# Kernel tuning notes

Hardware: AMD Instinct MI355X
Metric: run time of the kernel (lower is better)

The kernel has to match this reference:

```python
import jax, jax.numpy as jnp
import numpy as np

LN_EPS = 1e-5
NORM_EPS = 1e-12


def entmax15_last(x):
    """Exact 1.5-entmax over the last axis (Peters & Martins sort algorithm)."""
    d = x.shape[-1]
    x = x / 2.0
    x = x - jnp.max(x, axis=-1, keepdims=True)
    xs = jnp.sort(x, axis=-1)[..., ::-1]  # descending
    k = jnp.arange(1, d + 1, dtype=x.dtype)
    mean = jnp.cumsum(xs, axis=-1) / k
    meansq = jnp.cumsum(xs * xs, axis=-1) / k
    ss = k * (meansq - jnp.square(mean))
    delta = (1.0 - ss) / k
    tau = mean - jnp.sqrt(jnp.clip(delta, 0.0))
    support = (tau <= xs).astype(jnp.int32)
    k_star = jnp.sum(support, axis=-1, keepdims=True) - 1  # last valid index
    tau_star = jnp.take_along_axis(tau, k_star, axis=-1)
    return jnp.square(jnp.maximum(x - tau_star, 0.0))


def layer_norm(x, gamma, beta):
    mu = jnp.mean(x, axis=-1, keepdims=True)
    var = jnp.mean(jnp.square(x - mu), axis=-1, keepdims=True)
    return (x - mu) / jnp.sqrt(var + LN_EPS) * gamma + beta


def setup_inputs() -> dict:
    key = jax.random.key(0)
    ks = jax.random.split(key, 4)
    B, M, N, D, T, L = 256, 64, 32, 128, 64, 128
    return {
        "x": jax.random.normal(ks[0], (B, M, D), dtype=jnp.float32),
        "route_weights": jax.random.normal(ks[1], (M, N, D, T), dtype=jnp.float32),
        "thread": jax.random.uniform(ks[2], (1, M, N), dtype=jnp.float32),
        "routing_leaves": jax.random.uniform(ks[3], (L, T), dtype=jnp.float32),
        "ln_gamma": jnp.ones((T,), dtype=jnp.float32),
        "ln_beta": jnp.zeros((T,), dtype=jnp.float32),
    }


def reference(x, route_weights, thread, routing_leaves, ln_gamma, ln_beta):
    # entmax15 over dim=-2 (the in_capsule_size axis D) of route_weights [M,N,D,T]
    w = jnp.swapaxes(route_weights, -1, -2)
    w = entmax15_last(w)
    weights = jnp.swapaxes(w, -1, -2)
    # priors: [B, M, N, T]
    priors = jnp.einsum('bmd,mndt->bmnt', x, weights)
    # routing
    leave_hash = routing_leaves / jnp.maximum(
        jnp.linalg.norm(routing_leaves, axis=-1, keepdims=True), NORM_EPS)
    votes = jax.nn.sigmoid(jnp.einsum('ld,bmnt->bmnl', leave_hash, priors)) if False else \
        jax.nn.sigmoid(jnp.einsum('ld,bmnd->bmnl', leave_hash, priors))  # [B,M,N,L]
    mean_cap = jnp.mean(votes, axis=1, keepdims=True)
    dis = jnp.mean(jnp.square(votes - mean_cap), axis=-1)  # [B,M,N]
    weight = jax.nn.relu(jnp.square(thread) - dis)
    prob = jax.nn.softmax(weight, axis=-2)  # over M (in capsules)
    next_caps = jnp.sum(prob[:, :, :, None] * priors, axis=1)  # [B,N,T]
    return layer_norm(next_caps, ln_gamma, ln_beta)
```

## Files before the change

kernel.cpp:

```cpp
#include <hip/hip_runtime.h>
#include <hip/hip_bf16.h>
#include <math.h>

#define B_ 256
#define M_ 64
#define N_ 32
#define D_ 128
#define T_ 64
#define L_ 128

typedef __attribute__((ext_vector_type(8))) short short8;
typedef __attribute__((ext_vector_type(4))) float floatx4;

__device__ __forceinline__ unsigned short f2bf(float f) {
  unsigned int u = __float_as_uint(f);
  unsigned int r = (u + 0x7fffu + ((u >> 16) & 1u)) >> 16;
  return (unsigned short)r;
}
__device__ __forceinline__ float bf2f(unsigned short s) {
  return __uint_as_float(((unsigned int)s) << 16);
}
__device__ __forceinline__ float frcp(float x) { return __builtin_amdgcn_rcpf(x); }

__global__ __launch_bounds__(256) void k_entmax(const float* __restrict__ rw,
                                                unsigned short* __restrict__ wq2,
                                                const float* __restrict__ x,
                                                const float* __restrict__ leaves,
                                                unsigned short* __restrict__ xb2,
                                                unsigned short* __restrict__ lhn,
                                                const float* __restrict__ thr,
                                                float* __restrict__ thrT) {
  const int tid = threadIdx.x;
  if (blockIdx.x >= 2048) {
    int bid = blockIdx.x - 2048;
    if (bid < 2048) {
      size_t e = ((size_t)bid * 256 + tid) * 4;
      int b = (int)(e >> 13);
      int rem = (int)(e & 8191);
      int mm = rem >> 7, dd = rem & 127;
      float4 v = *(const float4*)(x + e);
      ushort4 o;
      o.x = f2bf(v.x); o.y = f2bf(v.y); o.z = f2bf(v.z); o.w = f2bf(v.w);
      *(ushort4*)(xb2 + ((size_t)mm * B_ + b) * D_ + dd) = o;
    } else if (bid == 2048) {
      if (tid < L_) {
        const float* r = leaves + tid * T_;
        float ss = 0.f;
        for (int i = 0; i < T_; ++i) ss = fmaf(r[i], r[i], ss);
        float inv = frcp(fmaxf(sqrtf(ss), 1e-12f));
        unsigned short* o = lhn + tid * T_;
        for (int i = 0; i < T_; ++i) o[i] = f2bf(r[i] * inv);
      }
    } else {
#pragma unroll
      for (int k = 0; k < 8; ++k) {
        int idx = k * 256 + tid;
        int nn = idx >> 6, mm = idx & 63;
        thrT[idx] = thr[mm * N_ + nn];
      }
    }
    return;
  }

  const int gv = blockIdx.x * 64 + (tid >> 2);
  const int h = tid & 3;
  const int mn = gv >> 6;
  const int t = gv & 63;
  const float* base = rw + ((size_t)mn * D_ + h * 32) * T_ + t;
  float xv_[32];
#pragma unroll
  for (int i = 0; i < 32; ++i) xv_[i] = base[(size_t)i * T_];
  float mx = xv_[0];
#pragma unroll
  for (int i = 1; i < 32; ++i) mx = fmaxf(mx, xv_[i]);
  mx = fmaxf(mx, __shfl_xor(mx, 1));
  mx = fmaxf(mx, __shfl_xor(mx, 2));
#pragma unroll
  for (int i = 0; i < 32; ++i) xv_[i] = (xv_[i] - mx) * 0.5f;

  float lo = -1.0f, hi = 0.0f;
  for (int it = 0; it < 12; ++it) {
    float tau = 0.5f * (lo + hi);
    float f0 = 0.0f, f1 = 0.0f;
#pragma unroll
    for (int i = 0; i < 16; ++i) {
      float u0 = fmaxf(xv_[2 * i] - tau, 0.0f);
      float u1 = fmaxf(xv_[2 * i + 1] - tau, 0.0f);
      f0 = fmaf(u0, u0, f0);
      f1 = fmaf(u1, u1, f1);
    }
    float f = f0 + f1;
    f += __shfl_xor(f, 1);
    f += __shfl_xor(f, 2);
    if (f >= 1.0f) lo = tau; else hi = tau;
  }
  float tau0 = 0.5f * (lo + hi);
  float cnt = 0.f, s1 = 0.f, s2 = 0.f;
#pragma unroll
  for (int i = 0; i < 32; ++i) {
    bool in = xv_[i] > tau0;
    float q = in ? xv_[i] : 0.0f;
    cnt += in ? 1.0f : 0.0f;
    s1 += q;
    s2 = fmaf(q, q, s2);
  }
  cnt += __shfl_xor(cnt, 1); cnt += __shfl_xor(cnt, 2);
  s1 += __shfl_xor(s1, 1);   s1 += __shfl_xor(s1, 2);
  s2 += __shfl_xor(s2, 1);   s2 += __shfl_xor(s2, 2);
  float rc = frcp(cnt);
  float mean = s1 * rc;
  float ss = s2 - mean * s1;
  float delta = (1.0f - ss) * rc;
  float tau = mean - sqrtf(fmaxf(delta, 0.0f));

  unsigned short pv[32];
#pragma unroll
  for (int i = 0; i < 32; ++i) {
    float u = fmaxf(xv_[i] - tau, 0.0f);
    pv[i] = f2bf(u * u);
  }
  uint4* o = (uint4*)(wq2 + (size_t)gv * D_ + h * 32);
#pragma unroll
  for (int j = 0; j < 4; ++j) {
    uint4 w;
    w.x = (unsigned)pv[8 * j + 0] | ((unsigned)pv[8 * j + 1] << 16);
    w.y = (unsigned)pv[8 * j + 2] | ((unsigned)pv[8 * j + 3] << 16);
    w.z = (unsigned)pv[8 * j + 4] | ((unsigned)pv[8 * j + 5] << 16);
    w.w = (unsigned)pv[8 * j + 6] | ((unsigned)pv[8 * j + 7] << 16);
    o[j] = w;
  }
}

#define BS_STRIDE 136
__global__ __launch_bounds__(256, 4) void k_priors(const unsigned short* __restrict__ xb2,
                                                   const unsigned short* __restrict__ wq2,
                                                   unsigned short* __restrict__ priors) {
  const int m = blockIdx.x, n = blockIdx.y;
  const int tid = threadIdx.x;
  const int wid = tid >> 6, lane = tid & 63;
  const int row16 = lane & 15, quad = lane >> 4;
  __shared__ __align__(16) unsigned short Bs[64 * BS_STRIDE];
  __shared__ __align__(16) unsigned short Ct[128 * 72];

  const unsigned short* bsrc = wq2 + ((size_t)(m * N_ + n) * T_) * D_;
  {
    int tr = tid >> 4;
    int c = tid & 15;
#pragma unroll
    for (int p = 0; p < 4; ++p) {
      int row = p * 16 + tr;
      uint4 v = *(const uint4*)(bsrc + row * D_ + c * 8);
      *(uint4*)&Bs[row * BS_STRIDE + c * 8] = v;
    }
  }
  __syncthreads();

#pragma unroll
  for (int c = 0; c < 2; ++c) {
    short8 afr[2][4];
#pragma unroll
    for (int sc = 0; sc < 2; ++sc) {
      const int brow = c * 128 + wid * 32 + sc * 16 + row16;
      const unsigned short* aptr = xb2 + ((size_t)m * B_ + brow) * D_ + quad * 8;
#pragma unroll
      for (int ks = 0; ks < 4; ++ks) afr[sc][ks] = *(const short8*)(aptr + ks * 32);
    }

    floatx4 acc[2][4];
#pragma unroll
    for (int sc = 0; sc < 2; ++sc)
#pragma unroll
      for (int cf = 0; cf < 4; ++cf) acc[sc][cf] = (floatx4){0.f, 0.f, 0.f, 0.f};

#pragma unroll
    for (int cf = 0; cf < 4; ++cf) {
#pragma unroll
      for (int ks = 0; ks < 4; ++ks) {
        short8 bfr = *(const short8*)&Bs[(cf * 16 + row16) * BS_STRIDE + ks * 32 + quad * 8];
#pragma unroll
        for (int sc = 0; sc < 2; ++sc)
          acc[sc][cf] = __builtin_amdgcn_mfma_f32_16x16x32_bf16(afr[sc][ks], bfr, acc[sc][cf], 0, 0, 0);
      }
    }

    if (c) __syncthreads();
#pragma unroll
    for (int sc = 0; sc < 2; ++sc)
#pragma unroll
      for (int cf = 0; cf < 4; ++cf)
#pragma unroll
        for (int r = 0; r < 4; ++r)
          Ct[(wid * 32 + sc * 16 + quad * 4 + r) * 72 + cf * 16 + row16] = f2bf(acc[sc][cf][r]);
    __syncthreads();

    {
      int q = tid >> 4, s = tid & 15;
      int row = q * 8 + (s >> 1);
      int half = s & 1;
      const unsigned short* src = &Ct[row * 72 + half * 32];
      unsigned short* dst = priors +
          ((((size_t)n * 32 + c * 16 + q) * M_ + m) * 8 + (s >> 1)) * T_ + half * 32;
      uint4 a0 = *(const uint4*)(src);
      uint4 a1 = *(const uint4*)(src + 8);
      uint4 a2 = *(const uint4*)(src + 16);
      uint4 a3 = *(const uint4*)(src + 24);
      *(uint4*)(dst) = a0;
      *(uint4*)(dst + 8) = a1;
      *(uint4*)(dst + 16) = a2;
      *(uint4*)(dst + 24) = a3;
    }
  }
}

__global__ __launch_bounds__(256, 4) void k_route(const unsigned short* __restrict__ priors,
                                                  const unsigned short* __restrict__ lhn,
                                                  const float* __restrict__ thrT,
                                                  const float* __restrict__ gamma,
                                                  const float* __restrict__ beta,
                                                  float* __restrict__ out) {
  const int n = blockIdx.x, g4 = blockIdx.y;
  const int tid = threadIdx.x;
  const int wid = tid >> 6, lane = tid & 63;
  const int col = lane & 15, quad = lane >> 4;

  __shared__ float probL[4][64];

  const int g = g4 >> 1;
  const int bq = (g4 & 1) * 4 + wid;

  const unsigned short* base = priors + (((size_t)n * 32 + g) * M_) * 512 + bq * T_;
  short8 afr[4][2];
#pragma unroll
  for (int mt = 0; mt < 4; ++mt)
#pragma unroll
    for (int ks = 0; ks < 2; ++ks)
      afr[mt][ks] = *(const short8*)(base + (size_t)(mt * 16 + col) * 512 + ks * 32 + quad * 8);

  float thv = thrT[n * 64 + lane];

  float dis[4][4];
#pragma unroll
  for (int mt = 0; mt < 4; ++mt)
#pragma unroll
    for (int r = 0; r < 4; ++r) dis[mt][r] = 0.f;

#pragma unroll
  for (int s4 = 0; s4 < 4; ++s4) {
    floatx4 acc[4][2];
#pragma unroll
    for (int mt = 0; mt < 4; ++mt)
#pragma unroll
      for (int lt = 0; lt < 2; ++lt) acc[mt][lt] = (floatx4){0.f, 0.f, 0.f, 0.f};

#pragma unroll
    for (int lt = 0; lt < 2; ++lt) {
#pragma unroll
      for (int ks = 0; ks < 2; ++ks) {
        short8 bfr = *(const short8*)(lhn + (s4 * 32 + lt * 16 + col) * T_ + ks * 32 + quad * 8);
#pragma unroll
        for (int mt = 0; mt < 4; ++mt)
          acc[mt][lt] = __builtin_amdgcn_mfma_f32_16x16x32_bf16(afr[mt][ks], bfr, acc[mt][lt], 0, 0, 0);
      }
    }

#pragma unroll
    for (int mt = 0; mt < 4; ++mt)
#pragma unroll
      for (int lt = 0; lt < 2; ++lt)
#pragma unroll
        for (int r = 0; r < 4; ++r)
          acc[mt][lt][r] = frcp(1.0f + __expf(-acc[mt][lt][r]));

    float mc[2];
#pragma unroll
    for (int lt = 0; lt < 2; ++lt) {
      float s = 0.f;
#pragma unroll
      for (int mt = 0; mt < 4; ++mt)
#pragma unroll
        for (int r = 0; r < 4; ++r) s += acc[mt][lt][r];
      s += __shfl_xor(s, 16);
      s += __shfl_xor(s, 32);
      mc[lt] = s * (1.0f / 64.0f);
    }

#pragma unroll
    for (int mt = 0; mt < 4; ++mt)
#pragma unroll
      for (int r = 0; r < 4; ++r) {
        float s = 0.f;
#pragma unroll
        for (int lt = 0; lt < 2; ++lt) {
          float df = acc[mt][lt][r] - mc[lt];
          s = fmaf(df, df, s);
        }
        dis[mt][r] += s;
      }
  }

#pragma unroll
  for (int off = 1; off <= 8; off <<= 1)
#pragma unroll
    for (int mt = 0; mt < 4; ++mt)
#pragma unroll
      for (int r = 0; r < 4; ++r) dis[mt][r] += __shfl_xor(dis[mt][r], off);

  float e[4][4];
  float mxw = 0.f;
#pragma unroll
  for (int mt = 0; mt < 4; ++mt)
#pragma unroll
    for (int r = 0; r < 4; ++r) {
      float th = __shfl(thv, mt * 16 + quad * 4 + r);
      float w = fmaxf(th * th - dis[mt][r] * (1.0f / 128.0f), 0.0f);
      e[mt][r] = w;
      mxw = fmaxf(mxw, w);
    }
  mxw = fmaxf(mxw, __shfl_xor(mxw, 16));
  mxw = fmaxf(mxw, __shfl_xor(mxw, 32));
  float ssum = 0.f;
#pragma unroll
  for (int mt = 0; mt < 4; ++mt)
#pragma unroll
    for (int r = 0; r < 4; ++r) {
      e[mt][r] = __expf(e[mt][r] - mxw);
      ssum += e[mt][r];
    }
  ssum += __shfl_xor(ssum, 16);
  ssum += __shfl_xor(ssum, 32);
  float inv = frcp(ssum);
  if (col == 0) {
#pragma unroll
    for (int mt = 0; mt < 4; ++mt)
#pragma unroll
      for (int r = 0; r < 4; ++r)
        probL[wid][mt * 16 + quad * 4 + r] = e[mt][r] * inv;
  }

  float pr[4];
#pragma unroll
  for (int mt = 0; mt < 4; ++mt) pr[mt] = probL[wid][mt * 16 + col];

  float o[2][8];
#pragma unroll
  for (int ks = 0; ks < 2; ++ks)
#pragma unroll
    for (int j = 0; j < 8; ++j) o[ks][j] = 0.f;
#pragma unroll
  for (int mt = 0; mt < 4; ++mt)
#pragma unroll
    for (int ks = 0; ks < 2; ++ks)
#pragma unroll
      for (int j = 0; j < 8; ++j)
        o[ks][j] = fmaf(pr[mt], bf2f((unsigned short)afr[mt][ks][j]), o[ks][j]);
#pragma unroll
  for (int off = 1; off <= 8; off <<= 1)
#pragma unroll
    for (int ks = 0; ks < 2; ++ks)
#pragma unroll
      for (int j = 0; j < 8; ++j) o[ks][j] += __shfl_xor(o[ks][j], off);

  float mu = 0.f;
#pragma unroll
  for (int ks = 0; ks < 2; ++ks)
#pragma unroll
    for (int j = 0; j < 8; ++j) mu += o[ks][j];
  mu += __shfl_xor(mu, 16);
  mu += __shfl_xor(mu, 32);
  mu *= (1.0f / 64.0f);
  float var = 0.f;
#pragma unroll
  for (int ks = 0; ks < 2; ++ks)
#pragma unroll
    for (int j = 0; j < 8; ++j) {
      float d = o[ks][j] - mu;
      o[ks][j] = d;
      var = fmaf(d, d, var);
    }
  var += __shfl_xor(var, 16);
  var += __shfl_xor(var, 32);
  var *= (1.0f / 64.0f);
  float rstd = rsqrtf(var + 1e-5f);

  if (col == 0) {
    const int b = g4 * 4 + wid;
    float* obase = out + ((size_t)b * N_ + n) * T_;
#pragma unroll
    for (int ks = 0; ks < 2; ++ks) {
      int tb = ks * 32 + quad * 8;
      float4 g0 = *(const float4*)(gamma + tb);
      float4 g1 = *(const float4*)(gamma + tb + 4);
      float4 b0 = *(const float4*)(beta + tb);
      float4 b1 = *(const float4*)(beta + tb + 4);
      float4 r0, r1;
      r0.x = o[ks][0] * rstd * g0.x + b0.x;
      r0.y = o[ks][1] * rstd * g0.y + b0.y;
      r0.z = o[ks][2] * rstd * g0.z + b0.z;
      r0.w = o[ks][3] * rstd * g0.w + b0.w;
      r1.x = o[ks][4] * rstd * g1.x + b1.x;
      r1.y = o[ks][5] * rstd * g1.y + b1.y;
      r1.z = o[ks][6] * rstd * g1.z + b1.z;
      r1.w = o[ks][7] * rstd * g1.w + b1.w;
      *(float4*)(obase + tb) = r0;
      *(float4*)(obase + tb + 4) = r1;
    }
  }
}

extern "C" void kernel_launch(void* const* d_in, const int* in_sizes, int n_in,
                              void* d_out, int out_size, void* d_ws, size_t ws_size,
                              hipStream_t stream) {
  const float* x = (const float*)d_in[0];
  const float* rw = (const float*)d_in[1];
  const float* thr = (const float*)d_in[2];
  const float* leaves = (const float*)d_in[3];
  const float* gamma = (const float*)d_in[4];
  const float* beta = (const float*)d_in[5];
  float* out = (float*)d_out;

  char* ws = (char*)d_ws;
  unsigned short* wq2 = (unsigned short*)(ws);
  unsigned short* priors = (unsigned short*)(ws + 33554432);
  unsigned short* xb2 = (unsigned short*)(ws + 33554432 + 67108864);
  unsigned short* lhn = (unsigned short*)(ws + 100663296 + 4194304);
  float* thrT = (float*)(ws + 104857600 + 16384);

  hipLaunchKernelGGL(k_entmax, dim3(4098), dim3(256), 0, stream, rw, wq2, x, leaves, xb2, lhn, thr, thrT);
  hipLaunchKernelGGL(k_priors, dim3(64, 32), dim3(256), 0, stream, xb2, wq2, priors);
  hipLaunchKernelGGL(k_route, dim3(32, 64), dim3(256), 0, stream, priors, lhn, thrT, gamma, beta, out);
}
```

Measured before the change: 194.0 us.

## Compute transposed priors MFMA to write output directly, drop LDS staging

The priors GEMM swaps its operand roles: the weights tile held in LDS becomes the A operand and x becomes B. Each lane's accumulator then holds four contiguous T values, which are stored straight to global memory as ushort4, removing the Ct shared-memory transpose buffer and its barriers. Dropping Ct lowers LDS use, so the occupancy hint rises from 4 to 6 blocks. Separately, the entmax bisection is cut from 12 to 10 iterations, which saves compute but leaves a coarser starting threshold for the refinement step that follows. The direct stores are 8-byte and scattered rather than 16-byte coalesced, which may hurt write efficiency.

```diff
diff --git a/kernel.cpp b/kernel.cpp
--- a/kernel.cpp
+++ b/kernel.cpp
@@ -79,7 +79,7 @@
   for (int i = 0; i < 32; ++i) xv_[i] = (xv_[i] - mx) * 0.5f;
 
   float lo = -1.0f, hi = 0.0f;
-  for (int it = 0; it < 12; ++it) {
+  for (int it = 0; it < 10; ++it) {
     float tau = 0.5f * (lo + hi);
     float f0 = 0.0f, f1 = 0.0f;
 #pragma unroll
@@ -132,7 +132,7 @@
 }
 
 #define BS_STRIDE 136
-__global__ __launch_bounds__(256, 4) void k_priors(const unsigned short* __restrict__ xb2,
+__global__ __launch_bounds__(256, 6) void k_priors(const unsigned short* __restrict__ xb2,
                                                    const unsigned short* __restrict__ wq2,
                                                    unsigned short* __restrict__ priors) {
   const int m = blockIdx.x, n = blockIdx.y;
@@ -140,7 +140,6 @@
   const int wid = tid >> 6, lane = tid & 63;
   const int row16 = lane & 15, quad = lane >> 4;
   __shared__ __align__(16) unsigned short Bs[64 * BS_STRIDE];
-  __shared__ __align__(16) unsigned short Ct[128 * 72];
 
   const unsigned short* bsrc = wq2 + ((size_t)(m * N_ + n) * T_) * D_;
   {
@@ -155,59 +154,29 @@
   }
   __syncthreads();
 
-#pragma unroll
-  for (int c = 0; c < 2; ++c) {
-    short8 afr[2][4];
-#pragma unroll
-    for (int sc = 0; sc < 2; ++sc) {
-      const int brow = c * 128 + wid * 32 + sc * 16 + row16;
-      const unsigned short* aptr = xb2 + ((size_t)m * B_ + brow) * D_ + quad * 8;
-#pragma unroll
-      for (int ks = 0; ks < 4; ++ks) afr[sc][ks] = *(const short8*)(aptr + ks * 32);
-    }
-
-    floatx4 acc[2][4];
-#pragma unroll
-    for (int sc = 0; sc < 2; ++sc)
-#pragma unroll
-      for (int cf = 0; cf < 4; ++cf) acc[sc][cf] = (floatx4){0.f, 0.f, 0.f, 0.f};
-
+  const int b = wid * 64 + row16;
+#pragma unroll
+  for (int sub = 0; sub < 4; ++sub) {
+    const int bb = b + sub * 16;
+    const unsigned short* xptr = xb2 + ((size_t)m * B_ + bb) * D_ + quad * 8;
+    short8 bfr[4];
+#pragma unroll
+    for (int ks = 0; ks < 4; ++ks) bfr[ks] = *(const short8*)(xptr + ks * 32);
+
+    unsigned short* dstb = priors +
+        ((((size_t)n * 32 + (bb >> 3)) * M_ + m) * 8 + (bb & 7)) * T_ + quad * 4;
 #pragma unroll
     for (int cf = 0; cf < 4; ++cf) {
+      floatx4 acc = (floatx4){0.f, 0.f, 0.f, 0.f};
 #pragma unroll
       for (int ks = 0; ks < 4; ++ks) {
-        short8 bfr = *(const short8*)&Bs[(cf * 16 + row16) * BS_STRIDE + ks * 32 + quad * 8];
-#pragma unroll
-        for (int sc = 0; sc < 2; ++sc)
-          acc[sc][cf] = __builtin_amdgcn_mfma_f32_16x16x32_bf16(afr[sc][ks], bfr, acc[sc][cf], 0, 0, 0);
+        short8 afr = *(const short8*)&Bs[(cf * 16 + row16) * BS_STRIDE + ks * 32 + quad * 8];
+        acc = __builtin_amdgcn_mfma_f32_16x16x32_bf16(afr, bfr[ks], acc, 0, 0, 0);
       }
-    }
-
-    if (c) __syncthreads();
-#pragma unroll
-    for (int sc = 0; sc < 2; ++sc)
-#pragma unroll
-      for (int cf = 0; cf < 4; ++cf)
-#pragma unroll
-        for (int r = 0; r < 4; ++r)
-          Ct[(wid * 32 + sc * 16 + quad * 4 + r) * 72 + cf * 16 + row16] = f2bf(acc[sc][cf][r]);
-    __syncthreads();
-
-    {
-      int q = tid >> 4, s = tid & 15;
-      int row = q * 8 + (s >> 1);
-      int half = s & 1;
-      const unsigned short* src = &Ct[row * 72 + half * 32];
-      unsigned short* dst = priors +
-          ((((size_t)n * 32 + c * 16 + q) * M_ + m) * 8 + (s >> 1)) * T_ + half * 32;
-      uint4 a0 = *(const uint4*)(src);
-      uint4 a1 = *(const uint4*)(src + 8);
-      uint4 a2 = *(const uint4*)(src + 16);
-      uint4 a3 = *(const uint4*)(src + 24);
-      *(uint4*)(dst) = a0;
-      *(uint4*)(dst + 8) = a1;
-      *(uint4*)(dst + 16) = a2;
-      *(uint4*)(dst + 24) = a3;
+      ushort4 o4;
+      o4.x = f2bf(acc[0]); o4.y = f2bf(acc[1]);
+      o4.z = f2bf(acc[2]); o4.w = f2bf(acc[3]);
+      *(ushort4*)(dstb + cf * 16) = o4;
     }
   }
 }
```

Measured after the change: 211.9 us. 1.09x slower.

## Vectorize entmax loads over T, permute x/wq2 layouts, swap MFMA operands in priors

Applied to the files above, without the earlier changes.

The entmax kernel now has each thread load float4 vectors across four adjacent T columns and handle 16 D values, with an 8-lane shuffle reduction. The bisection is cut from 12 to 10 iterations, and stores are packed 16-element bf16 runs. The x conversion and the D-index layout of wq2 are permuted to match, and k_priors swaps its grid to n-major, preloads all x fragments, and swaps MFMA operands so the epilogue writes ushort4 to LDS. This aims at coalesced global reads of route_weights and fewer scalar LDS stores, at the cost of more registers and a reordered D axis that must stay consistent between the two kernels.

```diff
diff --git a/kernel.cpp b/kernel.cpp
--- a/kernel.cpp
+++ b/kernel.cpp
@@ -31,18 +31,25 @@
                                                 const float* __restrict__ thr,
                                                 float* __restrict__ thrT) {
   const int tid = threadIdx.x;
-  if (blockIdx.x >= 2048) {
-    int bid = blockIdx.x - 2048;
-    if (bid < 2048) {
-      size_t e = ((size_t)bid * 256 + tid) * 4;
-      int b = (int)(e >> 13);
-      int rem = (int)(e & 8191);
-      int mm = rem >> 7, dd = rem & 127;
-      float4 v = *(const float4*)(x + e);
-      ushort4 o;
-      o.x = f2bf(v.x); o.y = f2bf(v.y); o.z = f2bf(v.z); o.w = f2bf(v.w);
-      *(ushort4*)(xb2 + ((size_t)mm * B_ + b) * D_ + dd) = o;
-    } else if (bid == 2048) {
+  const int bx = blockIdx.x;
+  if (bx >= 1024) {
+    int bid = bx - 1024;
+    if (bid < 512) {
+      int idx = bid * 256 + tid;
+      int j = idx & 7, b = (idx >> 3) & 255, m = idx >> 11;
+      const float* xs = x + ((size_t)b * M_ + m) * D_ + j;
+      unsigned short pv[16];
+#pragma unroll
+      for (int i = 0; i < 16; ++i) pv[i] = f2bf(xs[i * 8]);
+      unsigned short* dst = xb2 + ((size_t)m * B_ + b) * D_ + j * 16;
+      uint4 w0, w1;
+      w0.x = pv[0] | ((unsigned)pv[1] << 16);  w0.y = pv[2] | ((unsigned)pv[3] << 16);
+      w0.z = pv[4] | ((unsigned)pv[5] << 16);  w0.w = pv[6] | ((unsigned)pv[7] << 16);
+      w1.x = pv[8] | ((unsigned)pv[9] << 16);  w1.y = pv[10] | ((unsigned)pv[11] << 16);
+      w1.z = pv[12] | ((unsigned)pv[13] << 16); w1.w = pv[14] | ((unsigned)pv[15] << 16);
+      *(uint4*)(dst) = w0;
+      *(uint4*)(dst + 8) = w1;
+    } else if (bid == 512) {
       if (tid < L_) {
         const float* r = leaves + tid * T_;
         float ss = 0.f;
@@ -62,72 +69,102 @@
     return;
   }
 
-  const int gv = blockIdx.x * 64 + (tid >> 2);
-  const int h = tid & 3;
-  const int mn = gv >> 6;
-  const int t = gv & 63;
-  const float* base = rw + ((size_t)mn * D_ + h * 32) * T_ + t;
-  float xv_[32];
-#pragma unroll
-  for (int i = 0; i < 32; ++i) xv_[i] = base[(size_t)i * T_];
-  float mx = xv_[0];
-#pragma unroll
-  for (int i = 1; i < 32; ++i) mx = fmaxf(mx, xv_[i]);
-  mx = fmaxf(mx, __shfl_xor(mx, 1));
-  mx = fmaxf(mx, __shfl_xor(mx, 2));
-#pragma unroll
-  for (int i = 0; i < 32; ++i) xv_[i] = (xv_[i] - mx) * 0.5f;
-
-  float lo = -1.0f, hi = 0.0f;
-  for (int it = 0; it < 12; ++it) {
-    float tau = 0.5f * (lo + hi);
-    float f0 = 0.0f, f1 = 0.0f;
+  const int mn = bx * 2 + (tid >> 7);
+  const int sub = tid & 127;
+  const int g = sub >> 3;
+  const int j = sub & 7;
+  const float* base = rw + (size_t)mn * D_ * T_ + g * 4;
+
+  floatx4 xv[16];
+#pragma unroll
+  for (int i = 0; i < 16; ++i)
+    xv[i] = *(const floatx4*)(base + (size_t)(i * 8 + j) * T_);
+
+  floatx4 mx = xv[0];
+#pragma unroll
+  for (int i = 1; i < 16; ++i)
+#pragma unroll
+    for (int c = 0; c < 4; ++c) mx[c] = fmaxf(mx[c], xv[i][c]);
+#pragma unroll
+  for (int off = 1; off <= 4; off <<= 1)
+#pragma unroll
+    for (int c = 0; c < 4; ++c) mx[c] = fmaxf(mx[c], __shfl_xor(mx[c], off));
+#pragma unroll
+  for (int i = 0; i < 16; ++i)
+#pragma unroll
+    for (int c = 0; c < 4; ++c) xv[i][c] = (xv[i][c] - mx[c]) * 0.5f;
+
+  floatx4 lo = (floatx4){-1.f, -1.f, -1.f, -1.f};
+  floatx4 hi = (floatx4){0.f, 0.f, 0.f, 0.f};
+  for (int it = 0; it < 10; ++it) {
+    floatx4 tau, f = (floatx4){0.f, 0.f, 0.f, 0.f};
+#pragma unroll
+    for (int c = 0; c < 4; ++c) tau[c] = 0.5f * (lo[c] + hi[c]);
+#pragma unroll
+    for (int i = 0; i < 16; ++i)
+#pragma unroll
+      for (int c = 0; c < 4; ++c) {
+        float u = fmaxf(xv[i][c] - tau[c], 0.0f);
+        f[c] = fmaf(u, u, f[c]);
+      }
+#pragma unroll
+    for (int off = 1; off <= 4; off <<= 1)
+#pragma unroll
+      for (int c = 0; c < 4; ++c) f[c] += __shfl_xor(f[c], off);
+#pragma unroll
+    for (int c = 0; c < 4; ++c) {
+      bool ge = f[c] >= 1.0f;
+      lo[c] = ge ? tau[c] : lo[c];
+      hi[c] = ge ? hi[c] : tau[c];
+    }
+  }
+  floatx4 tau0, cnt = (floatx4){0,0,0,0}, s1 = (floatx4){0,0,0,0}, s2 = (floatx4){0,0,0,0};
+#pragma unroll
+  for (int c = 0; c < 4; ++c) tau0[c] = 0.5f * (lo[c] + hi[c]);
+#pragma unroll
+  for (int i = 0; i < 16; ++i)
+#pragma unroll
+    for (int c = 0; c < 4; ++c) {
+      bool in = xv[i][c] > tau0[c];
+      float q = in ? xv[i][c] : 0.0f;
+      cnt[c] += in ? 1.0f : 0.0f;
+      s1[c] += q;
+      s2[c] = fmaf(q, q, s2[c]);
+    }
+#pragma unroll
+  for (int off = 1; off <= 4; off <<= 1)
+#pragma unroll
+    for (int c = 0; c < 4; ++c) {
+      cnt[c] += __shfl_xor(cnt[c], off);
+      s1[c] += __shfl_xor(s1[c], off);
+      s2[c] += __shfl_xor(s2[c], off);
+    }
+  floatx4 tau;
+#pragma unroll
+  for (int c = 0; c < 4; ++c) {
+    float rc = frcp(cnt[c]);
+    float mean = s1[c] * rc;
+    float ss = s2[c] - mean * s1[c];
+    float delta = (1.0f - ss) * rc;
+    tau[c] = mean - sqrtf(fmaxf(delta, 0.0f));
+  }
+
+#pragma unroll
+  for (int c = 0; c < 4; ++c) {
+    unsigned short pv[16];
 #pragma unroll
     for (int i = 0; i < 16; ++i) {
-      float u0 = fmaxf(xv_[2 * i] - tau, 0.0f);
-      float u1 = fmaxf(xv_[2 * i + 1] - tau, 0.0f);
-      f0 = fmaf(u0, u0, f0);
-      f1 = fmaf(u1, u1, f1);
-    }
-    float f = f0 + f1;
-    f += __shfl_xor(f, 1);
-    f += __shfl_xor(f, 2);
-    if (f >= 1.0f) lo = tau; else hi = tau;
-  }
-  float tau0 = 0.5f * (lo + hi);
-  float cnt = 0.f, s1 = 0.f, s2 = 0.f;
-#pragma unroll
-  for (int i = 0; i < 32; ++i) {
-    bool in = xv_[i] > tau0;
-    float q = in ? xv_[i] : 0.0f;
-    cnt += in ? 1.0f : 0.0f;
-    s1 += q;
-    s2 = fmaf(q, q, s2);
-  }
-  cnt += __shfl_xor(cnt, 1); cnt += __shfl_xor(cnt, 2);
-  s1 += __shfl_xor(s1, 1);   s1 += __shfl_xor(s1, 2);
-  s2 += __shfl_xor(s2, 1);   s2 += __shfl_xor(s2, 2);
-  float rc = frcp(cnt);
-  float mean = s1 * rc;
-  float ss = s2 - mean * s1;
-  float delta = (1.0f - ss) * rc;
-  float tau = mean - sqrtf(fmaxf(delta, 0.0f));
-
-  unsigned short pv[32];
-#pragma unroll
-  for (int i = 0; i < 32; ++i) {
-    float u = fmaxf(xv_[i] - tau, 0.0f);
-    pv[i] = f2bf(u * u);
-  }
-  uint4* o = (uint4*)(wq2 + (size_t)gv * D_ + h * 32);
-#pragma unroll
-  for (int j = 0; j < 4; ++j) {
-    uint4 w;
-    w.x = (unsigned)pv[8 * j + 0] | ((unsigned)pv[8 * j + 1] << 16);
-    w.y = (unsigned)pv[8 * j + 2] | ((unsigned)pv[8 * j + 3] << 16);
-    w.z = (unsigned)pv[8 * j + 4] | ((unsigned)pv[8 * j + 5] << 16);
-    w.w = (unsigned)pv[8 * j + 6] | ((unsigned)pv[8 * j + 7] << 16);
-    o[j] = w;
+      float u = fmaxf(xv[i][c] - tau[c], 0.0f);
+      pv[i] = f2bf(u * u);
+    }
+    unsigned short* dst = wq2 + ((size_t)mn * 64 + g * 4 + c) * D_ + j * 16;
+    uint4 w0, w1;
+    w0.x = pv[0] | ((unsigned)pv[1] << 16);  w0.y = pv[2] | ((unsigned)pv[3] << 16);
+    w0.z = pv[4] | ((unsigned)pv[5] << 16);  w0.w = pv[6] | ((unsigned)pv[7] << 16);
+    w1.x = pv[8] | ((unsigned)pv[9] << 16);  w1.y = pv[10] | ((unsigned)pv[11] << 16);
+    w1.z = pv[12] | ((unsigned)pv[13] << 16); w1.w = pv[14] | ((unsigned)pv[15] << 16);
+    *(uint4*)(dst) = w0;
+    *(uint4*)(dst + 8) = w1;
   }
 }
 
@@ -135,62 +172,67 @@
 __global__ __launch_bounds__(256, 4) void k_priors(const unsigned short* __restrict__ xb2,
                                                    const unsigned short* __restrict__ wq2,
                                                    unsigned short* __restrict__ priors) {
-  const int m = blockIdx.x, n = blockIdx.y;
+  const int n = blockIdx.x, m = blockIdx.y;
   const int tid = threadIdx.x;
   const int wid = tid >> 6, lane = tid & 63;
   const int row16 = lane & 15, quad = lane >> 4;
   __shared__ __align__(16) unsigned short Bs[64 * BS_STRIDE];
   __shared__ __align__(16) unsigned short Ct[128 * 72];
 
-  const unsigned short* bsrc = wq2 + ((size_t)(m * N_ + n) * T_) * D_;
+  short8 xfr[2][2][4];
+#pragma unroll
+  for (int c = 0; c < 2; ++c)
+#pragma unroll
+    for (int sub = 0; sub < 2; ++sub) {
+      const int b = c * 128 + wid * 32 + sub * 16 + row16;
+      const unsigned short* xptr = xb2 + ((size_t)m * B_ + b) * D_ + quad * 8;
+#pragma unroll
+      for (int ks = 0; ks < 4; ++ks) xfr[c][sub][ks] = *(const short8*)(xptr + ks * 32);
+    }
+
   {
-    int tr = tid >> 4;
-    int c = tid & 15;
+    const unsigned short* bsrc = wq2 + ((size_t)(m * N_ + n) * T_) * D_;
+    int tr = tid >> 4, cc = tid & 15;
 #pragma unroll
     for (int p = 0; p < 4; ++p) {
       int row = p * 16 + tr;
-      uint4 v = *(const uint4*)(bsrc + row * D_ + c * 8);
-      *(uint4*)&Bs[row * BS_STRIDE + c * 8] = v;
+      uint4 v = *(const uint4*)(bsrc + row * D_ + cc * 8);
+      *(uint4*)&Bs[row * BS_STRIDE + cc * 8] = v;
     }
   }
   __syncthreads();
 
 #pragma unroll
   for (int c = 0; c < 2; ++c) {
-    short8 afr[2][4];
-#pragma unroll
-    for (int sc = 0; sc < 2; ++sc) {
-      const int brow = c * 128 + wid * 32 + sc * 16 + row16;
-      const unsigned short* aptr = xb2 + ((size_t)m * B_ + brow) * D_ + quad * 8;
-#pragma unroll
-      for (int ks = 0; ks < 4; ++ks) afr[sc][ks] = *(const short8*)(aptr + ks * 32);
-    }
-
     floatx4 acc[2][4];
 #pragma unroll
-    for (int sc = 0; sc < 2; ++sc)
-#pragma unroll
-      for (int cf = 0; cf < 4; ++cf) acc[sc][cf] = (floatx4){0.f, 0.f, 0.f, 0.f};
+    for (int sub = 0; sub < 2; ++sub)
+#pragma unroll
+      for (int cf = 0; cf < 4; ++cf) acc[sub][cf] = (floatx4){0.f, 0.f, 0.f, 0.f};
 
 #pragma unroll
     for (int cf = 0; cf < 4; ++cf) {
-#pragma unroll
-      for (int ks = 0; ks < 4; ++ks) {
-        short8 bfr = *(const short8*)&Bs[(cf * 16 + row16) * BS_STRIDE + ks * 32 + quad * 8];
-#pragma unroll
-        for (int sc = 0; sc < 2; ++sc)
-          acc[sc][cf] = __builtin_amdgcn_mfma_f32_16x16x32_bf16(afr[sc][ks], bfr, acc[sc][cf], 0, 0, 0);
-      }
+      short8 afr[4];
+#pragma unroll
+      for (int ks = 0; ks < 4; ++ks)
+        afr[ks] = *(const short8*)&Bs[(cf * 16 + row16) * BS_STRIDE + ks * 32 + quad * 8];
+#pragma unroll
+      for (int ks = 0; ks < 4; ++ks)
+#pragma unroll
+        for (int sub = 0; sub < 2; ++sub)
+          acc[sub][cf] = __builtin_amdgcn_mfma_f32_16x16x32_bf16(afr[ks], xfr[c][sub][ks], acc[sub][cf], 0, 0, 0);
     }
 
     if (c) __syncthreads();
 #pragma unroll
-    for (int sc = 0; sc < 2; ++sc)
-#pragma unroll
-      for (int cf = 0; cf < 4; ++cf)
-#pragma unroll
-        for (int r = 0; r < 4; ++r)
-          Ct[(wid * 32 + sc * 16 + quad * 4 + r) * 72 + cf * 16 + row16] = f2bf(acc[sc][cf][r]);
+    for (int sub = 0; sub < 2; ++sub)
+#pragma unroll
+      for (int cf = 0; cf < 4; ++cf) {
+        ushort4 o4;
+        o4.x = f2bf(acc[sub][cf][0]); o4.y = f2bf(acc[sub][cf][1]);
+        o4.z = f2bf(acc[sub][cf][2]); o4.w = f2bf(acc[sub][cf][3]);
+        *(ushort4*)&Ct[(wid * 32 + sub * 16 + row16) * 72 + cf * 16 + quad * 4] = o4;
+      }
     __syncthreads();
 
     {
@@ -425,7 +467,7 @@
   unsigned short* lhn = (unsigned short*)(ws + 100663296 + 4194304);
   float* thrT = (float*)(ws + 104857600 + 16384);
 
-  hipLaunchKernelGGL(k_entmax, dim3(4098), dim3(256), 0, stream, rw, wq2, x, leaves, xb2, lhn, thr, thrT);
-  hipLaunchKernelGGL(k_priors, dim3(64, 32), dim3(256), 0, stream, xb2, wq2, priors);
+  hipLaunchKernelGGL(k_entmax, dim3(1538), dim3(256), 0, stream, rw, wq2, x, leaves, xb2, lhn, thr, thrT);
+  hipLaunchKernelGGL(k_priors, dim3(32, 64), dim3(256), 0, stream, xb2, wq2, priors);
   hipLaunchKernelGGL(k_route, dim3(32, 64), dim3(256), 0, stream, priors, lhn, thrT, gamma, beta, out);
 }
```

Result: faster. 186.8 us (-3.7%).

## Fuse entmax into priors GEMM kernel and drop intermediate weight buffer

Applied to the files above, without the earlier changes.

The entmax computation moves from a separate kernel into the priors GEMM kernel. Each block loads its fp32 route_weights tile into LDS, runs entmax there and writes the bf16 weights straight into the MFMA B tile, so the 32MB bf16 weight buffer is no longer written to and re-read from global memory. The bisection count drops from 12 to 10 iterations, and the priors layout becomes [n][b][m][t] with vectorised Ct stores. In exchange the larger LDS footprint lowers occupancy to 3 blocks per CU, the GEMM operand roles are swapped, and the fewer iterations give a looser initial tau estimate before the exact refinement.

```diff
diff --git a/kernel.cpp b/kernel.cpp
--- a/kernel.cpp
+++ b/kernel.cpp
@@ -22,184 +22,183 @@
 }
 __device__ __forceinline__ float frcp(float x) { return __builtin_amdgcn_rcpf(x); }
 
-__global__ __launch_bounds__(256) void k_entmax(const float* __restrict__ rw,
-                                                unsigned short* __restrict__ wq2,
-                                                const float* __restrict__ x,
-                                                const float* __restrict__ leaves,
-                                                unsigned short* __restrict__ xb2,
-                                                unsigned short* __restrict__ lhn,
-                                                const float* __restrict__ thr,
-                                                float* __restrict__ thrT) {
+__global__ __launch_bounds__(256) void k_prep(const float* __restrict__ x,
+                                              const float* __restrict__ leaves,
+                                              unsigned short* __restrict__ xb2,
+                                              unsigned short* __restrict__ lhn,
+                                              const float* __restrict__ thr,
+                                              float* __restrict__ thrT) {
   const int tid = threadIdx.x;
-  if (blockIdx.x >= 2048) {
-    int bid = blockIdx.x - 2048;
-    if (bid < 2048) {
-      size_t e = ((size_t)bid * 256 + tid) * 4;
-      int b = (int)(e >> 13);
-      int rem = (int)(e & 8191);
-      int mm = rem >> 7, dd = rem & 127;
-      float4 v = *(const float4*)(x + e);
-      ushort4 o;
-      o.x = f2bf(v.x); o.y = f2bf(v.y); o.z = f2bf(v.z); o.w = f2bf(v.w);
-      *(ushort4*)(xb2 + ((size_t)mm * B_ + b) * D_ + dd) = o;
-    } else if (bid == 2048) {
-      if (tid < L_) {
-        const float* r = leaves + tid * T_;
-        float ss = 0.f;
-        for (int i = 0; i < T_; ++i) ss = fmaf(r[i], r[i], ss);
-        float inv = frcp(fmaxf(sqrtf(ss), 1e-12f));
-        unsigned short* o = lhn + tid * T_;
-        for (int i = 0; i < T_; ++i) o[i] = f2bf(r[i] * inv);
-      }
-    } else {
-#pragma unroll
-      for (int k = 0; k < 8; ++k) {
-        int idx = k * 256 + tid;
-        int nn = idx >> 6, mm = idx & 63;
-        thrT[idx] = thr[mm * N_ + nn];
-      }
-    }
-    return;
-  }
-
-  const int gv = blockIdx.x * 64 + (tid >> 2);
-  const int h = tid & 3;
-  const int mn = gv >> 6;
-  const int t = gv & 63;
-  const float* base = rw + ((size_t)mn * D_ + h * 32) * T_ + t;
-  float xv_[32];
-#pragma unroll
-  for (int i = 0; i < 32; ++i) xv_[i] = base[(size_t)i * T_];
-  float mx = xv_[0];
-#pragma unroll
-  for (int i = 1; i < 32; ++i) mx = fmaxf(mx, xv_[i]);
-  mx = fmaxf(mx, __shfl_xor(mx, 1));
-  mx = fmaxf(mx, __shfl_xor(mx, 2));
-#pragma unroll
-  for (int i = 0; i < 32; ++i) xv_[i] = (xv_[i] - mx) * 0.5f;
-
-  float lo = -1.0f, hi = 0.0f;
-  for (int it = 0; it < 12; ++it) {
-    float tau = 0.5f * (lo + hi);
-    float f0 = 0.0f, f1 = 0.0f;
-#pragma unroll
-    for (int i = 0; i < 16; ++i) {
-      float u0 = fmaxf(xv_[2 * i] - tau, 0.0f);
-      float u1 = fmaxf(xv_[2 * i + 1] - tau, 0.0f);
-      f0 = fmaf(u0, u0, f0);
-      f1 = fmaf(u1, u1, f1);
-    }
-    float f = f0 + f1;
-    f += __shfl_xor(f, 1);
-    f += __shfl_xor(f, 2);
-    if (f >= 1.0f) lo = tau; else hi = tau;
-  }
-  float tau0 = 0.5f * (lo + hi);
-  float cnt = 0.f, s1 = 0.f, s2 = 0.f;
-#pragma unroll
-  for (int i = 0; i < 32; ++i) {
-    bool in = xv_[i] > tau0;
-    float q = in ? xv_[i] : 0.0f;
-    cnt += in ? 1.0f : 0.0f;
-    s1 += q;
-    s2 = fmaf(q, q, s2);
-  }
-  cnt += __shfl_xor(cnt, 1); cnt += __shfl_xor(cnt, 2);
-  s1 += __shfl_xor(s1, 1);   s1 += __shfl_xor(s1, 2);
-  s2 += __shfl_xor(s2, 1);   s2 += __shfl_xor(s2, 2);
-  float rc = frcp(cnt);
-  float mean = s1 * rc;
-  float ss = s2 - mean * s1;
-  float delta = (1.0f - ss) * rc;
-  float tau = mean - sqrtf(fmaxf(delta, 0.0f));
-
-  unsigned short pv[32];
-#pragma unroll
-  for (int i = 0; i < 32; ++i) {
-    float u = fmaxf(xv_[i] - tau, 0.0f);
-    pv[i] = f2bf(u * u);
-  }
-  uint4* o = (uint4*)(wq2 + (size_t)gv * D_ + h * 32);
-#pragma unroll
-  for (int j = 0; j < 4; ++j) {
-    uint4 w;
-    w.x = (unsigned)pv[8 * j + 0] | ((unsigned)pv[8 * j + 1] << 16);
-    w.y = (unsigned)pv[8 * j + 2] | ((unsigned)pv[8 * j + 3] << 16);
-    w.z = (unsigned)pv[8 * j + 4] | ((unsigned)pv[8 * j + 5] << 16);
-    w.w = (unsigned)pv[8 * j + 6] | ((unsigned)pv[8 * j + 7] << 16);
-    o[j] = w;
+  const int bx = blockIdx.x;
+  if (bx < 2048) {
+    size_t e = ((size_t)bx * 256 + tid) * 4;
+    int b = (int)(e >> 13);
+    int rem = (int)(e & 8191);
+    int mm = rem >> 7, dd = rem & 127;
+    float4 v = *(const float4*)(x + e);
+    ushort4 o;
+    o.x = f2bf(v.x); o.y = f2bf(v.y); o.z = f2bf(v.z); o.w = f2bf(v.w);
+    *(ushort4*)(xb2 + ((size_t)mm * B_ + b) * D_ + dd) = o;
+  } else if (bx == 2048) {
+    if (tid < L_) {
+      const float* r = leaves + tid * T_;
+      float ss = 0.f;
+      for (int i = 0; i < T_; ++i) ss = fmaf(r[i], r[i], ss);
+      float inv = frcp(fmaxf(sqrtf(ss), 1e-12f));
+      unsigned short* o = lhn + tid * T_;
+      for (int i = 0; i < T_; ++i) o[i] = f2bf(r[i] * inv);
+    }
+  } else {
+#pragma unroll
+    for (int k = 0; k < 8; ++k) {
+      int idx = k * 256 + tid;
+      int nn = idx >> 6, mm = idx & 63;
+      thrT[idx] = thr[mm * N_ + nn];
+    }
   }
 }
 
 #define BS_STRIDE 136
-__global__ __launch_bounds__(256, 4) void k_priors(const unsigned short* __restrict__ xb2,
-                                                   const unsigned short* __restrict__ wq2,
-                                                   unsigned short* __restrict__ priors) {
+__global__ __launch_bounds__(256, 3) void k_wpriors(const unsigned short* __restrict__ xb2,
+                                                    const float* __restrict__ rw,
+                                                    unsigned short* __restrict__ priors) {
   const int m = blockIdx.x, n = blockIdx.y;
   const int tid = threadIdx.x;
   const int wid = tid >> 6, lane = tid & 63;
   const int row16 = lane & 15, quad = lane >> 4;
+
+  __shared__ __align__(16) float rwT[8192];
   __shared__ __align__(16) unsigned short Bs[64 * BS_STRIDE];
-  __shared__ __align__(16) unsigned short Ct[128 * 72];
-
-  const unsigned short* bsrc = wq2 + ((size_t)(m * N_ + n) * T_) * D_;
+  unsigned short* Ct = (unsigned short*)rwT;
+
+  short8 xfr[2][2][4];
+#pragma unroll
+  for (int c = 0; c < 2; ++c)
+#pragma unroll
+    for (int sub = 0; sub < 2; ++sub) {
+      const int b = c * 128 + wid * 32 + sub * 16 + row16;
+      const unsigned short* xptr = xb2 + ((size_t)m * B_ + b) * D_ + quad * 8;
+#pragma unroll
+      for (int ks = 0; ks < 4; ++ks) xfr[c][sub][ks] = *(const short8*)(xptr + ks * 32);
+    }
+
   {
-    int tr = tid >> 4;
-    int c = tid & 15;
-#pragma unroll
-    for (int p = 0; p < 4; ++p) {
-      int row = p * 16 + tr;
-      uint4 v = *(const uint4*)(bsrc + row * D_ + c * 8);
-      *(uint4*)&Bs[row * BS_STRIDE + c * 8] = v;
+    const float* src = rw + ((size_t)(m * N_ + n)) * (D_ * T_);
+#pragma unroll
+    for (int i = 0; i < 8; ++i) {
+      int idx = i * 256 + tid;
+      *(float4*)&rwT[idx * 4] = *(const float4*)(src + idx * 4);
     }
   }
   __syncthreads();
 
+  {
+    const int t = tid >> 2, q = tid & 3;
+    float xv[32];
+#pragma unroll
+    for (int i = 0; i < 32; ++i) xv[i] = rwT[(q * 32 + i) * 64 + t];
+    float mx = xv[0];
+#pragma unroll
+    for (int i = 1; i < 32; ++i) mx = fmaxf(mx, xv[i]);
+    mx = fmaxf(mx, __shfl_xor(mx, 1));
+    mx = fmaxf(mx, __shfl_xor(mx, 2));
+#pragma unroll
+    for (int i = 0; i < 32; ++i) xv[i] = (xv[i] - mx) * 0.5f;
+
+    float lo = -1.0f, hi = 0.0f;
+    for (int it = 0; it < 10; ++it) {
+      float tau = 0.5f * (lo + hi);
+      float f0 = 0.f, f1 = 0.f;
+#pragma unroll
+      for (int i = 0; i < 16; ++i) {
+        float u0 = fmaxf(xv[2 * i] - tau, 0.0f);
+        float u1 = fmaxf(xv[2 * i + 1] - tau, 0.0f);
+        f0 = fmaf(u0, u0, f0);
+        f1 = fmaf(u1, u1, f1);
+      }
+      float f = f0 + f1;
+      f += __shfl_xor(f, 1);
+      f += __shfl_xor(f, 2);
+      if (f >= 1.0f) lo = tau; else hi = tau;
+    }
+    float tau0 = 0.5f * (lo + hi);
+    float cnt = 0.f, s1 = 0.f, s2 = 0.f;
+#pragma unroll
+    for (int i = 0; i < 32; ++i) {
+      bool in = xv[i] > tau0;
+      float qv = in ? xv[i] : 0.0f;
+      cnt += in ? 1.0f : 0.0f;
+      s1 += qv;
+      s2 = fmaf(qv, qv, s2);
+    }
+    cnt += __shfl_xor(cnt, 1); cnt += __shfl_xor(cnt, 2);
+    s1 += __shfl_xor(s1, 1);   s1 += __shfl_xor(s1, 2);
+    s2 += __shfl_xor(s2, 1);   s2 += __shfl_xor(s2, 2);
+    float rc = frcp(cnt);
+    float mean = s1 * rc;
+    float ss = s2 - mean * s1;
+    float delta = (1.0f - ss) * rc;
+    float tau = mean - sqrtf(fmaxf(delta, 0.0f));
+
+    unsigned short pv[32];
+#pragma unroll
+    for (int i = 0; i < 32; ++i) {
+      float u = fmaxf(xv[i] - tau, 0.0f);
+      pv[i] = f2bf(u * u);
+    }
+    uint4* dst = (uint4*)&Bs[t * BS_STRIDE + q * 32];
+#pragma unroll
+    for (int j = 0; j < 4; ++j) {
+      uint4 w;
+      w.x = (unsigned)pv[8 * j + 0] | ((unsigned)pv[8 * j + 1] << 16);
+      w.y = (unsigned)pv[8 * j + 2] | ((unsigned)pv[8 * j + 3] << 16);
+      w.z = (unsigned)pv[8 * j + 4] | ((unsigned)pv[8 * j + 5] << 16);
+      w.w = (unsigned)pv[8 * j + 6] | ((unsigned)pv[8 * j + 7] << 16);
+      dst[j] = w;
+    }
+  }
+  __syncthreads();
+
 #pragma unroll
   for (int c = 0; c < 2; ++c) {
-    short8 afr[2][4];
-#pragma unroll
-    for (int sc = 0; sc < 2; ++sc) {
-      const int brow = c * 128 + wid * 32 + sc * 16 + row16;
-      const unsigned short* aptr = xb2 + ((size_t)m * B_ + brow) * D_ + quad * 8;
-#pragma unroll
-      for (int ks = 0; ks < 4; ++ks) afr[sc][ks] = *(const short8*)(aptr + ks * 32);
-    }
-
     floatx4 acc[2][4];
 #pragma unroll
-    for (int sc = 0; sc < 2; ++sc)
-#pragma unroll
-      for (int cf = 0; cf < 4; ++cf) acc[sc][cf] = (floatx4){0.f, 0.f, 0.f, 0.f};
+    for (int sub = 0; sub < 2; ++sub)
+#pragma unroll
+      for (int cf = 0; cf < 4; ++cf) acc[sub][cf] = (floatx4){0.f, 0.f, 0.f, 0.f};
 
 #pragma unroll
     for (int cf = 0; cf < 4; ++cf) {
-#pragma unroll
-      for (int ks = 0; ks < 4; ++ks) {
-        short8 bfr = *(const short8*)&Bs[(cf * 16 + row16) * BS_STRIDE + ks * 32 + quad * 8];
-#pragma unroll
-        for (int sc = 0; sc < 2; ++sc)
-          acc[sc][cf] = __builtin_amdgcn_mfma_f32_16x16x32_bf16(afr[sc][ks], bfr, acc[sc][cf], 0, 0, 0);
+      short8 afr[4];
+#pragma unroll
+      for (int ks = 0; ks < 4; ++ks)
+        afr[ks] = *(const short8*)&Bs[(cf * 16 + row16) * BS_STRIDE + ks * 32 + quad * 8];
+#pragma unroll
+      for (int ks = 0; ks < 4; ++ks)
+#pragma unroll
+        for (int sub = 0; sub < 2; ++sub)
+          acc[sub][cf] = __builtin_amdgcn_mfma_f32_16x16x32_bf16(afr[ks], xfr[c][sub][ks], acc[sub][cf], 0, 0, 0);
+    }
+
+    if (c) __syncthreads();
+#pragma unroll
+    for (int sub = 0; sub < 2; ++sub)
+#pragma unroll
+      for (int cf = 0; cf < 4; ++cf) {
+        ushort4 o4;
+        o4.x = f2bf(acc[sub][cf][0]); o4.y = f2bf(acc[sub][cf][1]);
+        o4.z = f2bf(acc[sub][cf][2]); o4.w = f2bf(acc[sub][cf][3]);
+        *(ushort4*)&Ct[(wid * 32 + sub * 16 + row16) * 72 + cf * 16 + quad * 4] = o4;
       }
-    }
-
-    if (c) __syncthreads();
-#pragma unroll
-    for (int sc = 0; sc < 2; ++sc)
-#pragma unroll
-      for (int cf = 0; cf < 4; ++cf)
-#pragma unroll
-        for (int r = 0; r < 4; ++r)
-          Ct[(wid * 32 + sc * 16 + quad * 4 + r) * 72 + cf * 16 + row16] = f2bf(acc[sc][cf][r]);
     __syncthreads();
 
     {
       int q = tid >> 4, s = tid & 15;
       int row = q * 8 + (s >> 1);
       int half = s & 1;
+      int b = c * 128 + row;
       const unsigned short* src = &Ct[row * 72 + half * 32];
-      unsigned short* dst = priors +
-          ((((size_t)n * 32 + c * 16 + q) * M_ + m) * 8 + (s >> 1)) * T_ + half * 32;
+      unsigned short* dst = priors + (((size_t)n * B_ + b) * M_ + m) * T_ + half * 32;
       uint4 a0 = *(const uint4*)(src);
       uint4 a1 = *(const uint4*)(src + 8);
       uint4 a2 = *(const uint4*)(src + 16);
@@ -225,16 +224,15 @@
 
   __shared__ float probL[4][64];
 
-  const int g = g4 >> 1;
-  const int bq = (g4 & 1) * 4 + wid;
-
-  const unsigned short* base = priors + (((size_t)n * 32 + g) * M_) * 512 + bq * T_;
+  const int b = g4 * 4 + wid;
+
+  const unsigned short* base = priors + ((size_t)n * B_ + b) * (M_ * T_);
   short8 afr[4][2];
 #pragma unroll
   for (int mt = 0; mt < 4; ++mt)
 #pragma unroll
     for (int ks = 0; ks < 2; ++ks)
-      afr[mt][ks] = *(const short8*)(base + (size_t)(mt * 16 + col) * 512 + ks * 32 + quad * 8);
+      afr[mt][ks] = *(const short8*)(base + (mt * 16 + col) * T_ + ks * 32 + quad * 8);
 
   float thv = thrT[n * 64 + lane];
 
@@ -383,7 +381,6 @@
   float rstd = rsqrtf(var + 1e-5f);
 
   if (col == 0) {
-    const int b = g4 * 4 + wid;
     float* obase = out + ((size_t)b * N_ + n) * T_;
 #pragma unroll
     for (int ks = 0; ks < 2; ++ks) {
@@ -419,13 +416,12 @@
   float* out = (float*)d_out;
 
   char* ws = (char*)d_ws;
-  unsigned short* wq2 = (unsigned short*)(ws);
-  unsigned short* priors = (unsigned short*)(ws + 33554432);
-  unsigned short* xb2 = (unsigned short*)(ws + 33554432 + 67108864);
-  unsigned short* lhn = (unsigned short*)(ws + 100663296 + 4194304);
-  float* thrT = (float*)(ws + 104857600 + 16384);
-
-  hipLaunchKernelGGL(k_entmax, dim3(4098), dim3(256), 0, stream, rw, wq2, x, leaves, xb2, lhn, thr, thrT);
-  hipLaunchKernelGGL(k_priors, dim3(64, 32), dim3(256), 0, stream, xb2, wq2, priors);
+  unsigned short* priors = (unsigned short*)(ws);
+  unsigned short* xb2 = (unsigned short*)(ws + 67108864);
+  unsigned short* lhn = (unsigned short*)(ws + 71303168);
+  float* thrT = (float*)(ws + 71319552);
+
+  hipLaunchKernelGGL(k_prep, dim3(2050), dim3(256), 0, stream, x, leaves, xb2, lhn, thr, thrT);
+  hipLaunchKernelGGL(k_wpriors, dim3(64, 32), dim3(256), 0, stream, xb2, rw, priors);
   hipLaunchKernelGGL(k_route, dim3(32, 64), dim3(256), 0, stream, priors, lhn, thrT, gamma, beta, out);
 }
```

New measurement: 178.6 us. -7.9%, faster.
